# Kernel optimization log

Measured on AMD Instinct MI355X. Metric: run time of the kernel, lower is better.

## Reference

```python
import math
import jax, jax.numpy as jnp
import numpy as np

N_HEADS = 16
CHUNK = 64  # sqrt(S) block size for the Cron-Root (sqrt-decomposition) branch


def _chunked_causal_attention(q, k, v, chunk=CHUNK):
    """Exact causal softmax attention computed in sqrt-size query blocks.

    Math-equivalent to F.scaled_dot_product_attention(q,k,v,is_causal=True),
    but never materializes the full [B,H,S,S] score matrix (honors the
    sqrt-decomposition structure of cron_root_attention_v14).
    q,k,v: [B,H,S,D] -> out [B,H,S,D]
    """
    B, H, S, D = q.shape
    scale = 1.0 / math.sqrt(D)
    nc = S // chunk
    qc = jnp.moveaxis(q.reshape(B, H, nc, chunk, D), 2, 0)  # [nc,B,H,C,D]
    kpos = jnp.arange(S)

    def body(_, inp):
        qi, ci = inp  # qi: [B,H,C,D], ci: scalar chunk index
        scores = jnp.einsum('bhcd,bhsd->bhcs', qi, k) * scale  # [B,H,C,S]
        qpos = ci * chunk + jnp.arange(chunk)
        mask = kpos[None, :] <= qpos[:, None]  # [C,S] causal
        scores = jnp.where(mask, scores, jnp.finfo(scores.dtype).min)
        p = jax.nn.softmax(scores, axis=-1)
        return None, jnp.einsum('bhcs,bhsd->bhcd', p, v)

    _, outs = jax.lax.scan(body, None, (qc, jnp.arange(nc)))  # [nc,B,H,C,D]
    return jnp.moveaxis(outs, 0, 2).reshape(B, H, S, D)


def setup_inputs() -> dict:
    key = jax.random.key(0)
    kx, kq, kk, kv, ko = jax.random.split(key, 5)
    d = 1024
    x = jax.random.normal(kx, (1, 4096, d), dtype=jnp.float32)
    # nn.Linear weights are [out_features, in_features]; no bias (bias=False)
    Wq = jax.random.normal(kq, (d, d), dtype=jnp.float32) * 0.02
    Wk = jax.random.normal(kk, (d, d), dtype=jnp.float32) * 0.02
    Wv = jax.random.normal(kv, (d, d), dtype=jnp.float32) * 0.02
    Wo = jax.random.normal(ko, (d, d), dtype=jnp.float32) * 0.02
    return {"x": x, "Wq": Wq, "Wk": Wk, "Wv": Wv, "Wo": Wo}


def reference(x, Wq, Wk, Wv, Wo):
    B, S, D = x.shape
    H = N_HEADS
    hd = D // H
    # projections (torch Linear: y = x @ W.T)
    q = (x @ Wq.T).reshape(B, S, H, hd).transpose(0, 2, 1, 3)
    k = (x @ Wk.T).reshape(B, S, H, hd).transpose(0, 2, 1, 3)
    v = (x @ Wv.T).reshape(B, S, H, hd).transpose(0, 2, 1, 3)
    # S=4096 >= threshold=1536 -> cron_root branch (exact causal attention)
    out = _chunked_causal_attention(q, k, v)
    out = out.transpose(0, 2, 1, 3).reshape(B, S, D)
    return out @ Wo.T
```

## Files before the change

### kernel.cpp

```cpp
#include <hip/hip_runtime.h>
#include <math.h>

#define S_LEN  4096
#define DMODEL 1024
#define NH     16
#define HD     64

typedef __bf16 bf16;
typedef __attribute__((ext_vector_type(8))) __bf16 bf16x8;
typedef __attribute__((ext_vector_type(4))) __bf16 bf16x4;
typedef __attribute__((ext_vector_type(4))) float  f32x4;

__device__ inline void gl_lds16(const void* g, void* l) {
    __builtin_amdgcn_global_load_lds(
        (const __attribute__((address_space(1))) void*)g,
        (__attribute__((address_space(3))) void*)l, 16, 0, 0);
}

__global__ __launch_bounds__(256)
void f32_to_bf16_all(const float* __restrict__ x,  const float* __restrict__ wq,
                     const float* __restrict__ wk, const float* __restrict__ wv,
                     const float* __restrict__ wo,
                     bf16* __restrict__ xb,  bf16* __restrict__ wqb,
                     bf16* __restrict__ wkb, bf16* __restrict__ wvb,
                     bf16* __restrict__ wob)
{
    int b = blockIdx.x;
    const float* s; bf16* d; int idx;
    if      (b < 2048) { s = x;  d = xb;  idx = b; }
    else if (b < 2560) { s = wq; d = wqb; idx = b - 2048; }
    else if (b < 3072) { s = wk; d = wkb; idx = b - 2560; }
    else if (b < 3584) { s = wv; d = wvb; idx = b - 3072; }
    else               { s = wo; d = wob; idx = b - 3584; }
    size_t e0 = ((size_t)idx * 256 + threadIdx.x) * 8;
    float4 a = *(const float4*)(s + e0);
    float4 c = *(const float4*)(s + e0 + 4);
    bf16x8 r;
    r[0] = (bf16)a.x; r[1] = (bf16)a.y; r[2] = (bf16)a.z; r[3] = (bf16)a.w;
    r[4] = (bf16)c.x; r[5] = (bf16)c.y; r[6] = (bf16)c.z; r[7] = (bf16)c.w;
    *(bf16x8*)(d + e0) = r;
}

template <typename OutT>
__device__ inline void gemm_body(const bf16* __restrict__ A, const bf16* __restrict__ B,
                                 OutT* __restrict__ C, bool trans, int M, int N, int K)
{
    __shared__ __align__(16) bf16 As[2][128 * 32];
    __shared__ __align__(16) bf16 Bs[2][128 * 32];

    const int t = threadIdx.x, lane = t & 63, w = t >> 6;
    const int m0 = blockIdx.x * 128, n0 = blockIdx.y * 128;
    const int wr = (w >> 1) * 64, wc = (w & 1) * 64;
    const int fr = lane & 15, fc = lane >> 4;

    const int  srow = w * 32 + (lane >> 2);
    const int  schk = (lane & 3) * 8;
    const bf16* Ag = A + (size_t)(m0 + srow) * K + schk;
    const bf16* Bg = B + (size_t)(n0 + srow) * K + schk;
    const int  sbase = (w * 32) * 32;

    f32x4 acc[4][4] = {};

    auto stage = [&](int buf, int k0) {
        gl_lds16(Ag + k0,                  &As[buf][sbase]);
        gl_lds16(Ag + k0 + (size_t)16 * K, &As[buf][sbase + 16 * 32]);
        gl_lds16(Bg + k0,                  &Bs[buf][sbase]);
        gl_lds16(Bg + k0 + (size_t)16 * K, &Bs[buf][sbase + 16 * 32]);
    };

    stage(0, 0);
    __syncthreads();
    int cur = 0;
    for (int k0 = 0; k0 < K; k0 += 32) {
        if (k0 + 32 < K) stage(cur ^ 1, k0 + 32);
        bf16x8 af[4], bv[4];
        #pragma unroll
        for (int fm = 0; fm < 4; ++fm)
            af[fm] = *(const bf16x8*)&As[cur][(wr + fm * 16 + fr) * 32 + fc * 8];
        #pragma unroll
        for (int fn = 0; fn < 4; ++fn)
            bv[fn] = *(const bf16x8*)&Bs[cur][(wc + fn * 16 + fr) * 32 + fc * 8];
        #pragma unroll
        for (int fm = 0; fm < 4; ++fm)
            #pragma unroll
            for (int fn = 0; fn < 4; ++fn)
                acc[fm][fn] = __builtin_amdgcn_mfma_f32_16x16x32_bf16(
                                  af[fm], bv[fn], acc[fm][fn], 0, 0, 0);
        __syncthreads();
        cur ^= 1;
    }

    #pragma unroll
    for (int fm = 0; fm < 4; ++fm)
        #pragma unroll
        for (int fn = 0; fn < 4; ++fn)
            #pragma unroll
            for (int r = 0; r < 4; ++r) {
                int row = m0 + wr + fm * 16 + fc * 4 + r;
                int col = n0 + wc + fn * 16 + fr;
                float v = acc[fm][fn][r];
                if (trans) C[(size_t)col * M + row] = (OutT)v;
                else       C[(size_t)row * N + col] = (OutT)v;
            }
}

__global__ __launch_bounds__(256)
void gemm_qkv(const bf16* __restrict__ A,
              const bf16* __restrict__ Wq, const bf16* __restrict__ Wk,
              const bf16* __restrict__ Wv,
              bf16* __restrict__ Qo, bf16* __restrict__ Ko, bf16* __restrict__ Vo)
{
    const int z = blockIdx.z;
    const bf16* B = (z == 0) ? Wq : (z == 1) ? Wk : Wv;
    bf16*       C = (z == 0) ? Qo : (z == 1) ? Ko : Vo;
    gemm_body<bf16>(A, B, C, z == 2, S_LEN, DMODEL, DMODEL);
}

__global__ __launch_bounds__(256)
void gemm_out(const bf16* __restrict__ A, const bf16* __restrict__ B,
              float* __restrict__ C)
{
    gemm_body<float>(A, B, C, false, S_LEN, DMODEL, DMODEL);
}

__global__ __launch_bounds__(256)
void attn_mfma(const bf16* __restrict__ Q, const bf16* __restrict__ Kb,
               const bf16* __restrict__ Vt, bf16* __restrict__ O)
{
    __shared__ __align__(16) bf16 Ks[2][64 * 64];
    __shared__ __align__(16) bf16 Vs[2][64 * 64];

    const int t = threadIdx.x, lane = t & 63, w = t >> 6;
    const int h  = blockIdx.x & (NH - 1);
    const int j  = (int)(blockIdx.x >> 4);
    const int a  = j & 15, sg = j >> 4;
    const int qi = (sg == 0) ? a : (sg == 1) ? 63 - a : (sg == 2) ? 16 + a : 47 - a;
    const int qbase = qi * 64;
    const int fr = lane & 15, fc = lane >> 4;

    bf16x8 qf[2];
    #pragma unroll
    for (int kh = 0; kh < 2; ++kh)
        qf[kh] = *(const bf16x8*)(Q + (size_t)(qbase + w * 16 + fr) * DMODEL
                                    + h * HD + kh * 32 + fc * 8);

    f32x4 o[4] = {};
    float lsum = 0.f;

    auto stage = [&](int buf, int kb2) {
        const int kbase2 = kb2 * 64;
        #pragma unroll
        for (int i = 0; i < 2; ++i) {
            int row = w * 16 + i * 8 + (lane >> 3);
            int gch = (lane & 7) ^ (row & 7);
            gl_lds16(Kb + (size_t)(kbase2 + row) * DMODEL + h * HD + gch * 8,
                     &Ks[buf][(w * 16 + i * 8) * 64]);
            gl_lds16(Vt + (size_t)(h * HD + row) * S_LEN + kbase2 + gch * 8,
                     &Vs[buf][(w * 16 + i * 8) * 64]);
        }
    };

    stage(0, 0);
    __syncthreads();

    int cur = 0;
    for (int kb = 0; kb <= qi; ++kb) {
        if (kb < qi) stage(cur ^ 1, kb + 1);

        f32x4 s[4] = {};
        #pragma unroll
        for (int fn = 0; fn < 4; ++fn)
            #pragma unroll
            for (int kh = 0; kh < 2; ++kh) {
                bf16x8 kf = *(const bf16x8*)
                    &Ks[cur][(fn * 16 + fr) * 64 + (((kh * 4 + fc) ^ (fr & 7)) * 8)];
                s[fn] = __builtin_amdgcn_mfma_f32_16x16x32_bf16(kf, qf[kh], s[fn], 0, 0, 0);
            }

        if (kb == qi) {
            #pragma unroll
            for (int fn = 0; fn < 4; ++fn)
                #pragma unroll
                for (int r = 0; r < 4; ++r)
                    if (fn * 16 + fc * 4 + r > w * 16 + fr) s[fn][r] = -INFINITY;
        }

        #pragma unroll
        for (int fn = 0; fn < 4; ++fn)
            #pragma unroll
            for (int r = 0; r < 4; ++r) {
                float p = exp2f(s[fn][r] * 0.18033688011112042f);
                lsum += p;
                s[fn][r] = p;
            }

        #pragma unroll
        for (int kvh = 0; kvh < 2; ++kvh) {
            bf16x8 pa;
            #pragma unroll
            for (int r = 0; r < 4; ++r) {
                pa[r]     = (bf16)s[2 * kvh][r];
                pa[4 + r] = (bf16)s[2 * kvh + 1][r];
            }
            #pragma unroll
            for (int fd = 0; fd < 4; ++fd) {
                const int rowb = (fd * 16 + fr) * 64 + (fc & 1) * 4;
                bf16x4 va = *(const bf16x4*)
                    &Vs[cur][rowb + (((kvh * 4     + (fc >> 1)) ^ (fr & 7)) * 8)];
                bf16x4 vb = *(const bf16x4*)
                    &Vs[cur][rowb + (((kvh * 4 + 2 + (fc >> 1)) ^ (fr & 7)) * 8)];
                bf16x8 vf;
                #pragma unroll
                for (int e = 0; e < 4; ++e) { vf[e] = va[e]; vf[4 + e] = vb[e]; }
                o[fd] = __builtin_amdgcn_mfma_f32_16x16x32_bf16(vf, pa, o[fd], 0, 0, 0);
            }
        }

        __syncthreads();
        cur ^= 1;
    }

    lsum += __shfl_xor(lsum, 16, 64);
    lsum += __shfl_xor(lsum, 32, 64);
    const float inv = 1.0f / lsum;

    #pragma unroll
    for (int fd = 0; fd < 4; ++fd) {
        bf16x4 ov;
        #pragma unroll
        for (int r = 0; r < 4; ++r) ov[r] = (bf16)(o[fd][r] * inv);
        *(bf16x4*)(O + (size_t)(qbase + w * 16 + fr) * DMODEL
                     + h * HD + fd * 16 + fc * 4) = ov;
    }
}

extern "C" void kernel_launch(void* const* d_in, const int* in_sizes, int n_in,
                              void* d_out, int out_size, void* d_ws, size_t ws_size,
                              hipStream_t stream)
{
    const float* x  = (const float*)d_in[0];
    const float* Wq = (const float*)d_in[1];
    const float* Wk = (const float*)d_in[2];
    const float* Wv = (const float*)d_in[3];
    const float* Wo = (const float*)d_in[4];

    const size_t M1 = 1024 * 1024;
    bf16* xb  = (bf16*)d_ws;
    bf16* wqb = xb  + 4 * M1;
    bf16* wkb = wqb + M1;
    bf16* wvb = wkb + M1;
    bf16* wob = wvb + M1;
    bf16* Qb  = wob + M1;
    bf16* Kb  = Qb  + 4 * M1;
    bf16* Vt  = Kb  + 4 * M1;
    bf16* Ob  = Vt  + 4 * M1;

    f32_to_bf16_all<<<4096, 256, 0, stream>>>(x, Wq, Wk, Wv, Wo,
                                              xb, wqb, wkb, wvb, wob);

    gemm_qkv<<<dim3(S_LEN / 128, DMODEL / 128, 3), 256, 0, stream>>>(
        xb, wqb, wkb, wvb, Qb, Kb, Vt);

    attn_mfma<<<dim3((S_LEN / 64) * NH), 256, 0, stream>>>(Qb, Kb, Vt, Ob);

    gemm_out<<<dim3(S_LEN / 128, DMODEL / 128), 256, 0, stream>>>(
        Ob, wob, (float*)d_out);
}
```

Measured before the change: 225.0 us.

## Pair complementary query blocks per attention workgroup to share K/V tiles

Each attention workgroup now handles two query blocks, i and 63-i, for the same head. The K/V tiles staged into LDS are reused by both. This balances causal work evenly across blocks and halves the grid, cutting redundant K/V global loads for the shorter block. In exchange it doubles accumulator and register pressure, adds branches on whether the short block is still active, and leaves only 512 workgroups to fill the GPU.

```diff
diff --git a/kernel.cpp b/kernel.cpp
--- a/kernel.cpp
+++ b/kernel.cpp
@@ -131,32 +131,35 @@
     __shared__ __align__(16) bf16 Vs[2][64 * 64];
 
     const int t = threadIdx.x, lane = t & 63, w = t >> 6;
-    const int h  = blockIdx.x & (NH - 1);
-    const int j  = (int)(blockIdx.x >> 4);
-    const int a  = j & 15, sg = j >> 4;
-    const int qi = (sg == 0) ? a : (sg == 1) ? 63 - a : (sg == 2) ? 16 + a : 47 - a;
-    const int qbase = qi * 64;
+    const int h = blockIdx.x & (NH - 1);
+    const int j = (int)(blockIdx.x >> 4);
+    const int i = (j < 16) ? j : 47 - j;
+    const int qiA = i, qiB = 63 - i;
+    const int qbA = qiA * 64, qbB = qiB * 64;
     const int fr = lane & 15, fc = lane >> 4;
 
-    bf16x8 qf[2];
+    bf16x8 qfA[2], qfB[2];
     #pragma unroll
-    for (int kh = 0; kh < 2; ++kh)
-        qf[kh] = *(const bf16x8*)(Q + (size_t)(qbase + w * 16 + fr) * DMODEL
-                                    + h * HD + kh * 32 + fc * 8);
-
-    f32x4 o[4] = {};
-    float lsum = 0.f;
+    for (int kh = 0; kh < 2; ++kh) {
+        qfA[kh] = *(const bf16x8*)(Q + (size_t)(qbA + w * 16 + fr) * DMODEL
+                                     + h * HD + kh * 32 + fc * 8);
+        qfB[kh] = *(const bf16x8*)(Q + (size_t)(qbB + w * 16 + fr) * DMODEL
+                                     + h * HD + kh * 32 + fc * 8);
+    }
+
+    f32x4 oA[4] = {}, oB[4] = {};
+    float lsA = 0.f, lsB = 0.f;
 
     auto stage = [&](int buf, int kb2) {
         const int kbase2 = kb2 * 64;
         #pragma unroll
-        for (int i = 0; i < 2; ++i) {
-            int row = w * 16 + i * 8 + (lane >> 3);
+        for (int ii = 0; ii < 2; ++ii) {
+            int row = w * 16 + ii * 8 + (lane >> 3);
             int gch = (lane & 7) ^ (row & 7);
             gl_lds16(Kb + (size_t)(kbase2 + row) * DMODEL + h * HD + gch * 8,
-                     &Ks[buf][(w * 16 + i * 8) * 64]);
+                     &Ks[buf][(w * 16 + ii * 8) * 64]);
             gl_lds16(Vt + (size_t)(h * HD + row) * S_LEN + kbase2 + gch * 8,
-                     &Vs[buf][(w * 16 + i * 8) * 64]);
+                     &Vs[buf][(w * 16 + ii * 8) * 64]);
         }
     };
 
@@ -164,44 +167,74 @@
     __syncthreads();
 
     int cur = 0;
-    for (int kb = 0; kb <= qi; ++kb) {
-        if (kb < qi) stage(cur ^ 1, kb + 1);
-
-        f32x4 s[4] = {};
+    #pragma unroll 2
+    for (int kb = 0; kb <= qiB; ++kb) {
+        if (kb < qiB) stage(cur ^ 1, kb + 1);
+        const bool actA = (kb <= qiA);
+
+        f32x4 sA[4] = {}, sB[4] = {};
         #pragma unroll
         for (int fn = 0; fn < 4; ++fn)
             #pragma unroll
             for (int kh = 0; kh < 2; ++kh) {
                 bf16x8 kf = *(const bf16x8*)
                     &Ks[cur][(fn * 16 + fr) * 64 + (((kh * 4 + fc) ^ (fr & 7)) * 8)];
-                s[fn] = __builtin_amdgcn_mfma_f32_16x16x32_bf16(kf, qf[kh], s[fn], 0, 0, 0);
-            }
-
-        if (kb == qi) {
+                if (actA)
+                    sA[fn] = __builtin_amdgcn_mfma_f32_16x16x32_bf16(kf, qfA[kh], sA[fn], 0, 0, 0);
+                sB[fn] = __builtin_amdgcn_mfma_f32_16x16x32_bf16(kf, qfB[kh], sB[fn], 0, 0, 0);
+            }
+
+        if (kb == qiA) {
             #pragma unroll
             for (int fn = 0; fn < 4; ++fn)
                 #pragma unroll
                 for (int r = 0; r < 4; ++r)
-                    if (fn * 16 + fc * 4 + r > w * 16 + fr) s[fn][r] = -INFINITY;
-        }
-
+                    if (fn * 16 + fc * 4 + r > w * 16 + fr) sA[fn][r] = -INFINITY;
+        }
+        if (kb == qiB) {
+            #pragma unroll
+            for (int fn = 0; fn < 4; ++fn)
+                #pragma unroll
+                for (int r = 0; r < 4; ++r)
+                    if (fn * 16 + fc * 4 + r > w * 16 + fr) sB[fn][r] = -INFINITY;
+        }
+
+        bf16x8 paA[2], paB[2];
+        if (actA) {
+            #pragma unroll
+            for (int fn = 0; fn < 4; ++fn)
+                #pragma unroll
+                for (int r = 0; r < 4; ++r) {
+                    float p = exp2f(sA[fn][r] * 0.18033688011112042f);
+                    lsA += p;
+                    sA[fn][r] = p;
+                }
+            #pragma unroll
+            for (int kvh = 0; kvh < 2; ++kvh)
+                #pragma unroll
+                for (int r = 0; r < 4; ++r) {
+                    paA[kvh][r]     = (bf16)sA[2 * kvh][r];
+                    paA[kvh][4 + r] = (bf16)sA[2 * kvh + 1][r];
+                }
+        }
         #pragma unroll
         for (int fn = 0; fn < 4; ++fn)
             #pragma unroll
             for (int r = 0; r < 4; ++r) {
-                float p = exp2f(s[fn][r] * 0.18033688011112042f);
-                lsum += p;
-                s[fn][r] = p;
-            }
-
-        #pragma unroll
-        for (int kvh = 0; kvh < 2; ++kvh) {
-            bf16x8 pa;
+                float p = exp2f(sB[fn][r] * 0.18033688011112042f);
+                lsB += p;
+                sB[fn][r] = p;
+            }
+        #pragma unroll
+        for (int kvh = 0; kvh < 2; ++kvh)
             #pragma unroll
             for (int r = 0; r < 4; ++r) {
-                pa[r]     = (bf16)s[2 * kvh][r];
-                pa[4 + r] = (bf16)s[2 * kvh + 1][r];
-            }
+                paB[kvh][r]     = (bf16)sB[2 * kvh][r];
+                paB[kvh][4 + r] = (bf16)sB[2 * kvh + 1][r];
+            }
+
+        #pragma unroll
+        for (int kvh = 0; kvh < 2; ++kvh)
             #pragma unroll
             for (int fd = 0; fd < 4; ++fd) {
                 const int rowb = (fd * 16 + fr) * 64 + (fc & 1) * 4;
@@ -212,25 +245,33 @@
                 bf16x8 vf;
                 #pragma unroll
                 for (int e = 0; e < 4; ++e) { vf[e] = va[e]; vf[4 + e] = vb[e]; }
-                o[fd] = __builtin_amdgcn_mfma_f32_16x16x32_bf16(vf, pa, o[fd], 0, 0, 0);
-            }
-        }
+                if (actA)
+                    oA[fd] = __builtin_amdgcn_mfma_f32_16x16x32_bf16(vf, paA[kvh], oA[fd], 0, 0, 0);
+                oB[fd] = __builtin_amdgcn_mfma_f32_16x16x32_bf16(vf, paB[kvh], oB[fd], 0, 0, 0);
+            }
 
         __syncthreads();
         cur ^= 1;
     }
 
-    lsum += __shfl_xor(lsum, 16, 64);
-    lsum += __shfl_xor(lsum, 32, 64);
-    const float inv = 1.0f / lsum;
+    lsA += __shfl_xor(lsA, 16, 64);
+    lsA += __shfl_xor(lsA, 32, 64);
+    lsB += __shfl_xor(lsB, 16, 64);
+    lsB += __shfl_xor(lsB, 32, 64);
+    const float invA = 1.0f / lsA, invB = 1.0f / lsB;
 
     #pragma unroll
     for (int fd = 0; fd < 4; ++fd) {
-        bf16x4 ov;
-        #pragma unroll
-        for (int r = 0; r < 4; ++r) ov[r] = (bf16)(o[fd][r] * inv);
-        *(bf16x4*)(O + (size_t)(qbase + w * 16 + fr) * DMODEL
-                     + h * HD + fd * 16 + fc * 4) = ov;
+        bf16x4 ovA, ovB;
+        #pragma unroll
+        for (int r = 0; r < 4; ++r) {
+            ovA[r] = (bf16)(oA[fd][r] * invA);
+            ovB[r] = (bf16)(oB[fd][r] * invB);
+        }
+        *(bf16x4*)(O + (size_t)(qbA + w * 16 + fr) * DMODEL
+                     + h * HD + fd * 16 + fc * 4) = ovA;
+        *(bf16x4*)(O + (size_t)(qbB + w * 16 + fr) * DMODEL
+                     + h * HD + fd * 16 + fc * 4) = ovB;
     }
 }
 
@@ -261,7 +302,7 @@
     gemm_qkv<<<dim3(S_LEN / 128, DMODEL / 128, 3), 256, 0, stream>>>(
         xb, wqb, wkb, wvb, Qb, Kb, Vt);
 
-    attn_mfma<<<dim3((S_LEN / 64) * NH), 256, 0, stream>>>(Qb, Kb, Vt, Ob);
+    attn_mfma<<<dim3((S_LEN / 64) * NH / 2), 256, 0, stream>>>(Qb, Kb, Vt, Ob);
 
     gemm_out<<<dim3(S_LEN / 128, DMODEL / 128), 256, 0, stream>>>(
         Ob, wob, (float*)d_out);
```

New measurement: 243.4 us. 8.2% more time.

## Pair causal query blocks per attention workgroup and halve GEMM N-tile

Applied to the files above, without the earlier changes.

Each attention workgroup now handles two query blocks (p and 63-p) in one 65-step loop. That gives every block equal causal work and halves the launch count, replacing the earlier interleaved block-order scheme. Partial results are normalized and written at each diagonal, after which the block switches to the second query. The GEMMs move from 128x128 to 128x64 tiles, doubling the grid size (256 to 512 blocks for the output GEMM) to fill the GPU better, at the cost of lower per-block data reuse. The attention grid drops to 512 workgroups, so occupancy may fall on a 256-CU part.

```diff
diff --git a/kernel.cpp b/kernel.cpp
--- a/kernel.cpp
+++ b/kernel.cpp
@@ -46,26 +46,27 @@
                                  OutT* __restrict__ C, bool trans, int M, int N, int K)
 {
     __shared__ __align__(16) bf16 As[2][128 * 32];
-    __shared__ __align__(16) bf16 Bs[2][128 * 32];
+    __shared__ __align__(16) bf16 Bs[2][64 * 32];
 
     const int t = threadIdx.x, lane = t & 63, w = t >> 6;
-    const int m0 = blockIdx.x * 128, n0 = blockIdx.y * 128;
-    const int wr = (w >> 1) * 64, wc = (w & 1) * 64;
+    const int m0 = blockIdx.x * 128, n0 = blockIdx.y * 64;
+    const int wr = (w >> 1) * 64, wc = (w & 1) * 32;
     const int fr = lane & 15, fc = lane >> 4;
 
-    const int  srow = w * 32 + (lane >> 2);
-    const int  schk = (lane & 3) * 8;
-    const bf16* Ag = A + (size_t)(m0 + srow) * K + schk;
-    const bf16* Bg = B + (size_t)(n0 + srow) * K + schk;
-    const int  sbase = (w * 32) * 32;
-
-    f32x4 acc[4][4] = {};
+    const int  srowA = w * 32 + (lane >> 2);
+    const int  srowB = w * 16 + (lane >> 2);
+    const int  schk  = (lane & 3) * 8;
+    const bf16* Ag = A + (size_t)(m0 + srowA) * K + schk;
+    const bf16* Bg = B + (size_t)(n0 + srowB) * K + schk;
+    const int  sbaseA = (w * 32) * 32;
+    const int  sbaseB = (w * 16) * 32;
+
+    f32x4 acc[4][2] = {};
 
     auto stage = [&](int buf, int k0) {
-        gl_lds16(Ag + k0,                  &As[buf][sbase]);
-        gl_lds16(Ag + k0 + (size_t)16 * K, &As[buf][sbase + 16 * 32]);
-        gl_lds16(Bg + k0,                  &Bs[buf][sbase]);
-        gl_lds16(Bg + k0 + (size_t)16 * K, &Bs[buf][sbase + 16 * 32]);
+        gl_lds16(Ag + k0,                  &As[buf][sbaseA]);
+        gl_lds16(Ag + k0 + (size_t)16 * K, &As[buf][sbaseA + 16 * 32]);
+        gl_lds16(Bg + k0,                  &Bs[buf][sbaseB]);
     };
 
     stage(0, 0);
@@ -73,17 +74,17 @@
     int cur = 0;
     for (int k0 = 0; k0 < K; k0 += 32) {
         if (k0 + 32 < K) stage(cur ^ 1, k0 + 32);
-        bf16x8 af[4], bv[4];
+        bf16x8 af[4], bv[2];
         #pragma unroll
         for (int fm = 0; fm < 4; ++fm)
             af[fm] = *(const bf16x8*)&As[cur][(wr + fm * 16 + fr) * 32 + fc * 8];
         #pragma unroll
-        for (int fn = 0; fn < 4; ++fn)
+        for (int fn = 0; fn < 2; ++fn)
             bv[fn] = *(const bf16x8*)&Bs[cur][(wc + fn * 16 + fr) * 32 + fc * 8];
         #pragma unroll
         for (int fm = 0; fm < 4; ++fm)
             #pragma unroll
-            for (int fn = 0; fn < 4; ++fn)
+            for (int fn = 0; fn < 2; ++fn)
                 acc[fm][fn] = __builtin_amdgcn_mfma_f32_16x16x32_bf16(
                                   af[fm], bv[fn], acc[fm][fn], 0, 0, 0);
         __syncthreads();
@@ -93,7 +94,7 @@
     #pragma unroll
     for (int fm = 0; fm < 4; ++fm)
         #pragma unroll
-        for (int fn = 0; fn < 4; ++fn)
+        for (int fn = 0; fn < 2; ++fn)
             #pragma unroll
             for (int r = 0; r < 4; ++r) {
                 int row = m0 + wr + fm * 16 + fc * 4 + r;
@@ -131,18 +132,19 @@
     __shared__ __align__(16) bf16 Vs[2][64 * 64];
 
     const int t = threadIdx.x, lane = t & 63, w = t >> 6;
-    const int h  = blockIdx.x & (NH - 1);
-    const int j  = (int)(blockIdx.x >> 4);
-    const int a  = j & 15, sg = j >> 4;
-    const int qi = (sg == 0) ? a : (sg == 1) ? 63 - a : (sg == 2) ? 16 + a : 47 - a;
-    const int qbase = qi * 64;
+    const int h   = blockIdx.x & (NH - 1);
+    const int p   = (int)(blockIdx.x >> 4);
+    const int qiA = p, qiB = 63 - p;
     const int fr = lane & 15, fc = lane >> 4;
 
-    bf16x8 qf[2];
+    bf16x8 qf[2], qfB[2];
     #pragma unroll
-    for (int kh = 0; kh < 2; ++kh)
-        qf[kh] = *(const bf16x8*)(Q + (size_t)(qbase + w * 16 + fr) * DMODEL
-                                    + h * HD + kh * 32 + fc * 8);
+    for (int kh = 0; kh < 2; ++kh) {
+        qf[kh]  = *(const bf16x8*)(Q + (size_t)(qiA * 64 + w * 16 + fr) * DMODEL
+                                     + h * HD + kh * 32 + fc * 8);
+        qfB[kh] = *(const bf16x8*)(Q + (size_t)(qiB * 64 + w * 16 + fr) * DMODEL
+                                     + h * HD + kh * 32 + fc * 8);
+    }
 
     f32x4 o[4] = {};
     float lsum = 0.f;
@@ -163,9 +165,13 @@
     stage(0, 0);
     __syncthreads();
 
-    int cur = 0;
-    for (int kb = 0; kb <= qi; ++kb) {
-        if (kb < qi) stage(cur ^ 1, kb + 1);
+    int cur = 0, qi_cur = qiA, qbase_cur = qiA * 64;
+    for (int tt = 0; tt < 65; ++tt) {
+        const int kv_local = (tt <= qiA) ? tt : tt - qiA - 1;
+        if (tt < 64) {
+            const int nkb = (tt + 1 <= qiA) ? tt + 1 : tt - qiA;
+            stage(cur ^ 1, nkb);
+        }
 
         f32x4 s[4] = {};
         #pragma unroll
@@ -177,7 +183,8 @@
                 s[fn] = __builtin_amdgcn_mfma_f32_16x16x32_bf16(kf, qf[kh], s[fn], 0, 0, 0);
             }
 
-        if (kb == qi) {
+        const bool diag = (kv_local == qi_cur);
+        if (diag) {
             #pragma unroll
             for (int fn = 0; fn < 4; ++fn)
                 #pragma unroll
@@ -189,9 +196,9 @@
         for (int fn = 0; fn < 4; ++fn)
             #pragma unroll
             for (int r = 0; r < 4; ++r) {
-                float p = exp2f(s[fn][r] * 0.18033688011112042f);
-                lsum += p;
-                s[fn][r] = p;
+                float pp = exp2f(s[fn][r] * 0.18033688011112042f);
+                lsum += pp;
+                s[fn][r] = pp;
             }
 
         #pragma unroll
@@ -216,21 +223,27 @@
             }
         }
 
+        if (diag) {
+            float ls = lsum;
+            ls += __shfl_xor(ls, 16, 64);
+            ls += __shfl_xor(ls, 32, 64);
+            const float inv = 1.0f / ls;
+            #pragma unroll
+            for (int fd = 0; fd < 4; ++fd) {
+                bf16x4 ov;
+                #pragma unroll
+                for (int r = 0; r < 4; ++r) ov[r] = (bf16)(o[fd][r] * inv);
+                *(bf16x4*)(O + (size_t)(qbase_cur + w * 16 + fr) * DMODEL
+                             + h * HD + fd * 16 + fc * 4) = ov;
+                o[fd] = (f32x4){0.f, 0.f, 0.f, 0.f};
+            }
+            lsum = 0.f;
+            qi_cur = qiB; qbase_cur = qiB * 64;
+            qf[0] = qfB[0]; qf[1] = qfB[1];
+        }
+
         __syncthreads();
         cur ^= 1;
-    }
-
-    lsum += __shfl_xor(lsum, 16, 64);
-    lsum += __shfl_xor(lsum, 32, 64);
-    const float inv = 1.0f / lsum;
-
-    #pragma unroll
-    for (int fd = 0; fd < 4; ++fd) {
-        bf16x4 ov;
-        #pragma unroll
-        for (int r = 0; r < 4; ++r) ov[r] = (bf16)(o[fd][r] * inv);
-        *(bf16x4*)(O + (size_t)(qbase + w * 16 + fr) * DMODEL
-                     + h * HD + fd * 16 + fc * 4) = ov;
     }
 }
 
@@ -258,11 +271,11 @@
     f32_to_bf16_all<<<4096, 256, 0, stream>>>(x, Wq, Wk, Wv, Wo,
                                               xb, wqb, wkb, wvb, wob);
 
-    gemm_qkv<<<dim3(S_LEN / 128, DMODEL / 128, 3), 256, 0, stream>>>(
+    gemm_qkv<<<dim3(S_LEN / 128, DMODEL / 64, 3), 256, 0, stream>>>(
         xb, wqb, wkb, wvb, Qb, Kb, Vt);
 
-    attn_mfma<<<dim3((S_LEN / 64) * NH), 256, 0, stream>>>(Qb, Kb, Vt, Ob);
-
-    gemm_out<<<dim3(S_LEN / 128, DMODEL / 128), 256, 0, stream>>>(
+    attn_mfma<<<dim3((S_LEN / 64) * NH / 2), 256, 0, stream>>>(Qb, Kb, Vt, Ob);
+
+    gemm_out<<<dim3(S_LEN / 128, DMODEL / 64), 256, 0, stream>>>(
         Ob, wob, (float*)d_out);
 }
```

Result: slower. 235.7 us (+4.8%).
